# Optimization experiments

Hardware: AMD Instinct MI355X
Metric: run time of the kernel (lower is better)

## Reference

```python
import jax, jax.numpy as jnp
import numpy as np


def setup_inputs() -> dict:
    key = jax.random.key(0)
    ks = jax.random.split(key, 10)
    T, D, E, K, H = 16384, 1024, 8, 2, 4096
    scale = 0.02
    return {
        "x_flat": jax.random.normal(ks[0], (T, D), jnp.float32),
        "noise": jax.random.normal(ks[1], (T, E), jnp.float32),
        "gate_w": jax.random.normal(ks[2], (E, D), jnp.float32) * scale,
        "noise_weight": jnp.zeros((E,), jnp.float32),
        "w1": jax.random.normal(ks[3], (E, H, D), jnp.float32) * scale,
        "b1": jnp.zeros((E, H), jnp.float32),
        "w2": jax.random.normal(ks[4], (E, H, D), jnp.float32) * scale,
        "b2": jnp.zeros((E, H), jnp.float32),
        "wp": jax.random.normal(ks[5], (E, D, H), jnp.float32) * scale,
        "bp": jnp.zeros((E, D), jnp.float32),
    }


K_TOP = 2
LOAD_BALANCE_SCALE = 0.01


def reference(x_flat, noise, gate_w, noise_weight, w1, b1, w2, b2, wp, bp):
    T, D = x_flat.shape
    E = gate_w.shape[0]
    # ---- gate ----
    logits = x_flat @ gate_w.T                        # [T, E]
    gate_weights = jax.nn.softmax(logits, axis=-1)    # [T, E]
    gw_mean = gate_weights.mean(axis=0)               # [E]
    uniform = jnp.ones_like(gw_mean) / E
    load_balance_loss = jnp.mean((gw_mean - uniform) ** 2) * LOAD_BALANCE_SCALE
    # noisy top-k (noise_weight initialized to zeros => noise is a no-op, kept for faithfulness)
    logits_noisy = logits + noise * noise_weight
    top_v, top_i = jax.lax.top_k(logits_noisy, K_TOP)  # [T, K]
    neg_inf = jnp.full_like(logits_noisy, -jnp.inf)
    sparse = neg_inf.at[jnp.arange(T)[:, None], top_i].set(top_v)
    top_k_gated_weights = jax.nn.softmax(sparse, axis=-1)  # [T, E], zero off top-k
    # ---- experts (SwiGLU), weighted combine ----
    # Non-top-k weights are exactly 0, so a dense masked sum over experts equals
    # the original gather/grouped-GEMM/scatter dispatch on a single device.
    y = jnp.zeros_like(x_flat)
    for e in range(E):
        h = x_flat @ w1[e].T + b1[e]                  # [T, H]
        g = jax.nn.silu(x_flat @ w2[e].T + b2[e])     # [T, H]
        out_e = (h * g) @ wp[e].T + bp[e]             # [T, D]
        y = y + top_k_gated_weights[:, e:e + 1] * out_e
    return y, load_balance_loss
```

## Files before the change

kernel.cpp:

```cpp
#include <hip/hip_runtime.h>
#include <hip/hip_bf16.h>

#define T_TOK 16384
#define DDIM  1024
#define NEXP  8
#define HDIM  4096
#define HQ    1024
#define NQ    4
#define TOTR  (2 * T_TOK)

#define BM 128
#define BK 64

typedef __attribute__((ext_vector_type(8))) short bf16x8;
typedef __attribute__((ext_vector_type(4))) float f32x4;

__device__ __forceinline__ unsigned short f2bf(float f) {
  unsigned int x = __builtin_bit_cast(unsigned int, f);
  x += 0x7fffu + ((x >> 16) & 1u);
  return (unsigned short)(x >> 16);
}
__device__ __forceinline__ void gload16(void* lds, const void* g) {
  __builtin_amdgcn_global_load_lds(
      (const __attribute__((address_space(1))) unsigned int*)g,
      (__attribute__((address_space(3))) unsigned int*)lds, 16, 0, 0);
}
__device__ __forceinline__ f32x4 mfma16(bf16x8 a, bf16x8 b, f32x4 c) {
  return __builtin_amdgcn_mfma_f32_16x16x32_bf16(a, b, c, 0, 0, 0);
}

#define OFF_GWSUM  ((size_t)0)
#define OFF_OFF16  ((size_t)64)
#define OFF_NP     ((size_t)128)
#define OFF_BLK    ((size_t)1024)
#define OFF_GBASE  ((size_t)8192)
#define OFF_PEXPP  ((size_t)16384)
#define OFF_PM0P   ((size_t)18432)
#define OFF_PENDP  ((size_t)20480)
#define OFF_PEXPS  ((size_t)22528)
#define OFF_PM0S   ((size_t)24576)
#define OFF_PENDS  ((size_t)26624)
#define OFF_TOPE   ((size_t)32768)
#define OFF_TOPW   (OFF_TOPE   + (size_t)T_TOK*2*4)
#define OFF_LRANK  (OFF_TOPW   + (size_t)T_TOK*2*4)
#define OFF_ROWTOK (OFF_LRANK  + (size_t)T_TOK*4)
#define OFF_ROWG   (OFF_ROWTOK + (size_t)T_TOK*2*4)
#define OFF_XG     ((size_t)1 << 20)
#define OFF_ACTQ   (OFF_XG   + (size_t)TOTR*DDIM*2)
#define OFF_W1Q    (OFF_ACTQ + (size_t)TOTR*HQ*2)
#define OFF_W2Q    (OFF_W1Q  + (size_t)NEXP*HQ*DDIM*2)
#define OFF_WPQ    (OFF_W2Q  + (size_t)NEXP*HQ*DDIM*2)
#define WS_NEEDED  (OFF_WPQ  + (size_t)NEXP*DDIM*HQ*2 + ((size_t)1<<20))

__global__ __launch_bounds__(256) void k_gate(
    const float* __restrict__ x, const float* __restrict__ noise,
    const float* __restrict__ gate_w, const float* __restrict__ nw,
    float* __restrict__ gwsum, int* __restrict__ tope, float* __restrict__ topw)
{
  __shared__ float gw_s[NEXP * DDIM];
  __shared__ float blk_gw[NEXP];
  const int tid = threadIdx.x;
  if (tid < NEXP) blk_gw[tid] = 0.f;
  {
    float4* dst = (float4*)gw_s;
    const float4* src = (const float4*)gate_w;
    for (int i = tid; i < NEXP * DDIM / 4; i += 256) dst[i] = src[i];
  }
  __syncthreads();

  const int wv = tid >> 6, lane = tid & 63;
  const int t = blockIdx.x * 4 + wv;

  const float4* xr = (const float4*)(x + (size_t)t * DDIM);
  float4 xv[4];
  #pragma unroll
  for (int c = 0; c < 4; ++c) xv[c] = xr[lane + 64 * c];

  float logit[NEXP];
  #pragma unroll
  for (int e = 0; e < NEXP; ++e) {
    float p = 0.f;
    const float4* g4 = (const float4*)(gw_s + e * DDIM);
    #pragma unroll
    for (int c = 0; c < 4; ++c) {
      float4 g = g4[lane + 64 * c];
      p += xv[c].x * g.x + xv[c].y * g.y + xv[c].z * g.z + xv[c].w * g.w;
    }
    #pragma unroll
    for (int off = 32; off >= 1; off >>= 1) p += __shfl_xor(p, off, 64);
    logit[e] = p;
  }

  if (lane == 0) {
    float m = logit[0];
    #pragma unroll
    for (int e = 1; e < NEXP; ++e) m = fmaxf(m, logit[e]);
    float sm[NEXP]; float s = 0.f;
    #pragma unroll
    for (int e = 0; e < NEXP; ++e) { sm[e] = expf(logit[e] - m); s += sm[e]; }
    float inv = 1.f / s;
    #pragma unroll
    for (int e = 0; e < NEXP; ++e) atomicAdd(&blk_gw[e], sm[e] * inv);

    float ln[NEXP];
    #pragma unroll
    for (int e = 0; e < NEXP; ++e) ln[e] = logit[e] + noise[(size_t)t * NEXP + e] * nw[e];
    int i1 = 0; float v1 = ln[0];
    #pragma unroll
    for (int e = 1; e < NEXP; ++e) if (ln[e] > v1) { v1 = ln[e]; i1 = e; }
    int i2 = -1; float v2 = -3.4e38f;
    #pragma unroll
    for (int e = 0; e < NEXP; ++e) if (e != i1 && ln[e] > v2) { v2 = ln[e]; i2 = e; }
    float b = expf(v2 - v1);
    float wsum = 1.f + b;
    tope[2 * t] = i1; tope[2 * t + 1] = i2;
    topw[2 * t] = 1.f / wsum; topw[2 * t + 1] = b / wsum;
  }
  __syncthreads();
  if (tid < NEXP) atomicAdd(&gwsum[tid], blk_gw[tid]);
}

__global__ __launch_bounds__(256) void k_hist(
    const int* __restrict__ tope, unsigned int* __restrict__ lrank,
    int* __restrict__ blkcnt)
{
  __shared__ int cnt16[16];
  const int tid = threadIdx.x;
  const int t = blockIdx.x * 256 + tid;
  if (tid < 16) cnt16[tid] = 0;
  __syncthreads();
  const int e0 = tope[2 * t], e1 = tope[2 * t + 1];
  const int b0 = 2 * e0 + (e0 < e1 ? 0 : 1);
  const int b1 = 2 * e1 + (e1 < e0 ? 0 : 1);
  const int lr0 = atomicAdd(&cnt16[b0], 1);
  const int lr1 = atomicAdd(&cnt16[b1], 1);
  lrank[t] = (unsigned int)lr0 | ((unsigned int)lr1 << 16);
  __syncthreads();
  if (tid < 16) blkcnt[blockIdx.x * 16 + tid] = cnt16[tid];
}

__global__ __launch_bounds__(512) void k_scan(
    const int* __restrict__ blkcnt, int* __restrict__ gbase,
    int* __restrict__ off16, int* __restrict__ np,
    int* __restrict__ pexpP, int* __restrict__ pm0P, int* __restrict__ pendP,
    int* __restrict__ pexpS, int* __restrict__ pm0S, int* __restrict__ pendS,
    const float* __restrict__ gwsum, float* __restrict__ out_loss)
{
  __shared__ int ld[64][16];
  __shared__ int sc[64][16];
  __shared__ int tot[16];
  __shared__ int o16[16];
  const int tid = threadIdx.x;
  for (int i = tid; i < 1024; i += 512) ld[i >> 4][i & 15] = blkcnt[i];
  __syncthreads();
  if (tid < 16) {
    int run = 0;
    for (int i = 0; i < 64; ++i) { sc[i][tid] = run; run += ld[i][tid]; }
    tot[tid] = run;
  }
  __syncthreads();
  if (tid == 0) {
    int o = 0;
    for (int b = 0; b < 16; ++b) { o16[b] = o; off16[b] = o; o += tot[b]; }
    int nP = 0, nS = 0;
    for (int b = 0; b < 16; ++b) {
      const int e = b >> 1, s = b & 1;
      const int beg = o16[b], end = beg + tot[b];
      for (int m = beg; m < end; m += BM) {
        const int me = (m + BM < end) ? (m + BM) : end;
        if (!s) { pexpP[nP] = e; pm0P[nP] = m; pendP[nP] = me; ++nP; }
        else    { pexpS[nS] = e; pm0S[nS] = m; pendS[nS] = me; ++nS; }
      }
    }
    np[0] = nP; np[1] = nS;
    float s = 0.f;
    for (int i = 0; i < NEXP; ++i) {
      float d = gwsum[i] / (float)T_TOK - 1.f / (float)NEXP;
      s += d * d;
    }
    out_loss[0] = (s / (float)NEXP) * 0.01f;
  }
  __syncthreads();
  for (int i = tid; i < 1024; i += 512)
    gbase[i] = o16[i & 15] + sc[i >> 4][i & 15];
}

__global__ __launch_bounds__(256) void k_copy(
    const float* __restrict__ x, const int* __restrict__ tope,
    const float* __restrict__ topw, const unsigned int* __restrict__ lrank,
    const int* __restrict__ gbase,
    int* __restrict__ rowtok, float* __restrict__ rowgate,
    unsigned short* __restrict__ Xg)
{
  const int tid = threadIdx.x;
  const int wv = tid >> 6, lane = tid & 63;
  const int t = blockIdx.x * 4 + wv;
  const int e0 = tope[2 * t], e1 = tope[2 * t + 1];
  const int b0 = 2 * e0 + (e0 < e1 ? 0 : 1);
  const int b1 = 2 * e1 + (e1 < e0 ? 0 : 1);
  const unsigned int lr = lrank[t];
  const int hb = t >> 8;
  const int r0 = gbase[hb * 16 + b0] + (int)(lr & 0xffffu);
  const int r1 = gbase[hb * 16 + b1] + (int)(lr >> 16);
  if (lane == 0) {
    rowtok[r0] = t; rowtok[r1] = t;
    rowgate[r0] = topw[2 * t]; rowgate[r1] = topw[2 * t + 1];
  }
  const float4* xr = (const float4*)(x + (size_t)t * DDIM);
  ushort4 o[4];
  #pragma unroll
  for (int c = 0; c < 4; ++c) {
    float4 v = xr[lane + 64 * c];
    o[c].x = f2bf(v.x); o[c].y = f2bf(v.y); o[c].z = f2bf(v.z); o[c].w = f2bf(v.w);
  }
  ushort4* d0 = (ushort4*)(Xg + (size_t)r0 * DDIM);
  ushort4* d1 = (ushort4*)(Xg + (size_t)r1 * DDIM);
  #pragma unroll
  for (int c = 0; c < 4; ++c) d0[lane + 64 * c] = o[c];
  #pragma unroll
  for (int c = 0; c < 4; ++c) d1[lane + 64 * c] = o[c];
}

__global__ __launch_bounds__(256) void k_castall(
    const float* __restrict__ w1, const float* __restrict__ w2,
    const float* __restrict__ wp,
    unsigned short* __restrict__ w1q, unsigned short* __restrict__ w2q,
    unsigned short* __restrict__ wpq, int q)
{
  const int N4 = NEXP * HQ * DDIM / 4;
  for (int i = blockIdx.x * 256 + threadIdx.x; i < 3 * N4; i += gridDim.x * 256) {
    int j = i;
    float4 v; size_t dstIdx; unsigned short* d;
    if (j < N4) {
      const int c4 = j & 255, rr = j >> 8, e = rr >> 10, r = rr & 1023;
      v = ((const float4*)w1)[((size_t)e * HDIM + q * HQ + r) * 256 + c4];
      d = w1q; dstIdx = (size_t)rr * 256 + c4;
    } else if (j < 2 * N4) {
      j -= N4;
      const int c4 = j & 255, rr = j >> 8, e = rr >> 10, r = rr & 1023;
      v = ((const float4*)w2)[((size_t)e * HDIM + q * HQ + r) * 256 + c4];
      d = w2q; dstIdx = (size_t)rr * 256 + c4;
    } else {
      j -= 2 * N4;
      const int c4 = j & 255, rr = j >> 8;
      v = ((const float4*)wp)[(size_t)rr * 1024 + q * 256 + c4];
      d = wpq; dstIdx = (size_t)rr * 256 + c4;
    }
    ushort4 o;
    o.x = f2bf(v.x); o.y = f2bf(v.y); o.z = f2bf(v.z); o.w = f2bf(v.w);
    ((ushort4*)d)[dstIdx] = o;
  }
}

#define FBN 64
#define FGX 280
#define FGY 16
__global__ __launch_bounds__(256, 2) void k_fused(
    const unsigned short* __restrict__ Xg,
    const unsigned short* __restrict__ w1q, const unsigned short* __restrict__ w2q,
    const float* __restrict__ b1, const float* __restrict__ b2,
    unsigned short* __restrict__ actq, const int* __restrict__ np,
    const int* __restrict__ pexpP, const int* __restrict__ pm0P, const int* __restrict__ pendP,
    const int* __restrict__ pexpS, const int* __restrict__ pm0S, const int* __restrict__ pendS,
    int q)
{
  const int flat = blockIdx.y * FGX + blockIdx.x;
  const int CPX = (FGX * FGY) / 8;
  const int L = (flat & 7) * CPX + (flat >> 3);
  const int pidx = L >> 4;
  const int yc = L & 15;
  const int nP = np[0], nS = np[1];
  int e, m0, mend;
  if (pidx < nP)            { e = pexpP[pidx]; m0 = pm0P[pidx]; mend = pendP[pidx]; }
  else if (pidx < nP + nS)  { int s = pidx - nP; e = pexpS[s]; m0 = pm0S[s]; mend = pendS[s]; }
  else return;

  __shared__ unsigned short As[2][BM * BK];
  __shared__ unsigned short B1s[2][FBN * BK];
  __shared__ unsigned short B2s[2][FBN * BK];

  const int tid = threadIdx.x;
  const int wid = tid >> 6, lane = tid & 63;
  const int wr = wid >> 1, wc = wid & 1;
  const int fr = lane & 15;
  const int fq = lane >> 4;

  const unsigned short* Bbase1 = w1q + ((size_t)e * HQ + yc * FBN) * DDIM;
  const unsigned short* Bbase2 = w2q + ((size_t)e * HQ + yc * FBN) * DDIM;

  f32x4 acc1[4][2] = {};
  f32x4 acc2[4][2] = {};

  auto stage = [&](int kt, int cur) {
    const int k0 = kt * BK;
    #pragma unroll
    for (int it = 0; it < 4; ++it) {
      const int idx = it * 256 + tid;
      const int row = idx >> 3, seg = idx & 7;
      const int koff = ((seg ^ (row & 7)) << 3);
      int arow = m0 + row; if (arow >= TOTR) arow = TOTR - 1;
      gload16(&As[cur][idx * 8], Xg + (size_t)arow * DDIM + k0 + koff);
    }
    #pragma unroll
    for (int it = 0; it < 2; ++it) {
      const int idx = it * 256 + tid;
      const int row = idx >> 3, seg = idx & 7;
      const int koff = ((seg ^ (row & 7)) << 3);
      gload16(&B1s[cur][idx * 8], Bbase1 + (size_t)row * DDIM + k0 + koff);
    }
    #pragma unroll
    for (int it = 0; it < 2; ++it) {
      const int idx = it * 256 + tid;
      const int row = idx >> 3, seg = idx & 7;
      const int koff = ((seg ^ (row & 7)) << 3);
      gload16(&B2s[cur][idx * 8], Bbase2 + (size_t)row * DDIM + k0 + koff);
    }
  };

  const int NSTEP = DDIM / BK;
  stage(0, 0);

  for (int kt = 0; kt < NSTEP; ++kt) {
    const int cur = kt & 1;
    const bool has_next = (kt + 1 < NSTEP);
    if (has_next) stage(kt + 1, cur ^ 1);
    if (has_next) asm volatile("s_waitcnt vmcnt(8)" ::: "memory");
    else          asm volatile("s_waitcnt vmcnt(0)" ::: "memory");
    __builtin_amdgcn_sched_barrier(0);
    __builtin_amdgcn_s_barrier();
    __builtin_amdgcn_s_setprio(1);

    #pragma unroll
    for (int kk = 0; kk < 2; ++kk) {
      bf16x8 b1v[2], b2v[2];
      #pragma unroll
      for (int nf = 0; nf < 2; ++nf) {
        const int row = wc * 32 + nf * 16 + fr;
        const int seg = (kk * 4 + fq) ^ (row & 7);
        b1v[nf] = *(const bf16x8*)&B1s[cur][row * BK + seg * 8];
        b2v[nf] = *(const bf16x8*)&B2s[cur][row * BK + seg * 8];
      }
      #pragma unroll
      for (int mf = 0; mf < 4; ++mf) {
        const int row = wr * 64 + mf * 16 + fr;
        const int seg = (kk * 4 + fq) ^ (row & 7);
        bf16x8 av = *(const bf16x8*)&As[cur][row * BK + seg * 8];
        #pragma unroll
        for (int nf = 0; nf < 2; ++nf) {
          acc1[mf][nf] = mfma16(av, b1v[nf], acc1[mf][nf]);
          acc2[mf][nf] = mfma16(av, b2v[nf], acc2[mf][nf]);
        }
      }
    }

    __builtin_amdgcn_s_setprio(0);
    __builtin_amdgcn_s_barrier();
    __builtin_amdgcn_sched_barrier(0);
  }

  const int mcnt = mend - m0;
  #pragma unroll
  for (int mf = 0; mf < 4; ++mf) {
    const int rb = wr * 64 + mf * 16 + (fq << 2);
    #pragma unroll
    for (int nf = 0; nf < 2; ++nf) {
      const int cq = yc * FBN + wc * 32 + nf * 16 + fr;
      const float bb1 = b1[(size_t)e * HDIM + q * HQ + cq];
      const float bb2 = b2[(size_t)e * HDIM + q * HQ + cq];
      #pragma unroll
      for (int j = 0; j < 4; ++j) {
        const int lr = rb + j;
        if (lr < mcnt) {
          float h = acc1[mf][nf][j] + bb1;
          float g = acc2[mf][nf][j] + bb2;
          float s = g / (1.f + expf(-g));
          actq[(size_t)(m0 + lr) * HQ + cq] = f2bf(h * s);
        }
      }
    }
  }
}

#define DBN 64
#define DGX 144
#define DGY 16
template<bool STORE>
__global__ __launch_bounds__(256, 2) void k_down(
    const unsigned short* __restrict__ actq, const unsigned short* __restrict__ wpq,
    const float* __restrict__ bp,
    const int* __restrict__ np, int npIdx,
    const int* __restrict__ pexp, const int* __restrict__ pm0, const int* __restrict__ pend,
    const int* __restrict__ rowtok, const float* __restrict__ rowgate,
    float* __restrict__ Y)
{
  const int flat = blockIdx.y * DGX + blockIdx.x;
  const int CPX = (DGX * DGY) / 8;
  const int L = (flat & 7) * CPX + (flat >> 3);
  const int pidx = L >> 4;
  const int yc = L & 15;
  if (pidx >= np[npIdx]) return;
  const int e = pexp[pidx], m0 = pm0[pidx], mend = pend[pidx];

  __shared__ unsigned short As[2][BM * BK];
  __shared__ unsigned short Bs[2][DBN * BK];

  const int tid = threadIdx.x;
  const int wid = tid >> 6, lane = tid & 63;
  const int wr = wid >> 1, wc = wid & 1;
  const int fr = lane & 15;
  const int fq = lane >> 4;

  const unsigned short* Bbase = wpq + ((size_t)e * DDIM + yc * DBN) * HQ;

  f32x4 acc[4][2] = {};

  auto stage = [&](int kt, int cur) {
    const int k0 = kt * BK;
    #pragma unroll
    for (int it = 0; it < 4; ++it) {
      const int idx = it * 256 + tid;
      const int row = idx >> 3, seg = idx & 7;
      const int koff = ((seg ^ (row & 7)) << 3);
      int arow = m0 + row; if (arow >= TOTR) arow = TOTR - 1;
      gload16(&As[cur][idx * 8], actq + (size_t)arow * HQ + k0 + koff);
    }
    #pragma unroll
    for (int it = 0; it < 2; ++it) {
      const int idx = it * 256 + tid;
      const int row = idx >> 3, seg = idx & 7;
      const int koff = ((seg ^ (row & 7)) << 3);
      gload16(&Bs[cur][idx * 8], Bbase + (size_t)row * HQ + k0 + koff);
    }
  };

  const int NSTEP = HQ / BK;
  stage(0, 0);

  for (int kt = 0; kt < NSTEP; ++kt) {
    const int cur = kt & 1;
    const bool has_next = (kt + 1 < NSTEP);
    if (has_next) stage(kt + 1, cur ^ 1);
    if (has_next) asm volatile("s_waitcnt vmcnt(6)" ::: "memory");
    else          asm volatile("s_waitcnt vmcnt(0)" ::: "memory");
    __builtin_amdgcn_sched_barrier(0);
    __builtin_amdgcn_s_barrier();
    __builtin_amdgcn_s_setprio(1);

    #pragma unroll
    for (int kk = 0; kk < 2; ++kk) {
      bf16x8 bv[2];
      #pragma unroll
      for (int nf = 0; nf < 2; ++nf) {
        const int row = wc * 32 + nf * 16 + fr;
        const int seg = (kk * 4 + fq) ^ (row & 7);
        bv[nf] = *(const bf16x8*)&Bs[cur][row * BK + seg * 8];
      }
      #pragma unroll
      for (int mf = 0; mf < 4; ++mf) {
        const int row = wr * 64 + mf * 16 + fr;
        const int seg = (kk * 4 + fq) ^ (row & 7);
        bf16x8 av = *(const bf16x8*)&As[cur][row * BK + seg * 8];
        #pragma unroll
        for (int nf = 0; nf < 2; ++nf)
          acc[mf][nf] = mfma16(av, bv[nf], acc[mf][nf]);
      }
    }

    __builtin_amdgcn_s_setprio(0);
    __builtin_amdgcn_s_barrier();
    __builtin_amdgcn_sched_barrier(0);
  }

  const int mcnt = mend - m0;
  #pragma unroll
  for (int mf = 0; mf < 4; ++mf) {
    const int rb = wr * 64 + mf * 16 + (fq << 2);
    #pragma unroll
    for (int nf = 0; nf < 2; ++nf) {
      const int dg = yc * DBN + wc * 32 + nf * 16 + fr;
      const float bb = bp[(size_t)e * DDIM + dg];
      #pragma unroll
      for (int j = 0; j < 4; ++j) {
        const int lr = rb + j;
        if (lr < mcnt) {
          const int r = m0 + lr;
          const float o = rowgate[r] * (acc[mf][nf][j] + bb);
          float* yp = &Y[(size_t)rowtok[r] * DDIM + dg];
          if (STORE) *yp = o; else *yp += o;
        }
      }
    }
  }
}

extern "C" void kernel_launch(void* const* d_in, const int* in_sizes, int n_in,
                              void* d_out, int out_size, void* d_ws, size_t ws_size,
                              hipStream_t stream) {
  const float* x      = (const float*)d_in[0];
  const float* noise  = (const float*)d_in[1];
  const float* gate_w = (const float*)d_in[2];
  const float* nw     = (const float*)d_in[3];
  const float* w1     = (const float*)d_in[4];
  const float* b1     = (const float*)d_in[5];
  const float* w2     = (const float*)d_in[6];
  const float* b2     = (const float*)d_in[7];
  const float* wp     = (const float*)d_in[8];
  const float* bp     = (const float*)d_in[9];
  float* y = (float*)d_out;

  if (ws_size < WS_NEEDED) return;

  char* ws = (char*)d_ws;
  float* gwsum   = (float*)(ws + OFF_GWSUM);
  int*   off16   = (int*)(ws + OFF_OFF16);
  int*   np      = (int*)(ws + OFF_NP);
  int*   blkcnt  = (int*)(ws + OFF_BLK);
  int*   gbase   = (int*)(ws + OFF_GBASE);
  int*   pexpP   = (int*)(ws + OFF_PEXPP);
  int*   pm0P    = (int*)(ws + OFF_PM0P);
  int*   pendP   = (int*)(ws + OFF_PENDP);
  int*   pexpS   = (int*)(ws + OFF_PEXPS);
  int*   pm0S    = (int*)(ws + OFF_PM0S);
  int*   pendS   = (int*)(ws + OFF_PENDS);
  int*   tope    = (int*)(ws + OFF_TOPE);
  float* topw    = (float*)(ws + OFF_TOPW);
  unsigned int* lrank = (unsigned int*)(ws + OFF_LRANK);
  int*   rowtok  = (int*)(ws + OFF_ROWTOK);
  float* rowgate = (float*)(ws + OFF_ROWG);
  unsigned short* Xg   = (unsigned short*)(ws + OFF_XG);
  unsigned short* actq = (unsigned short*)(ws + OFF_ACTQ);
  unsigned short* w1q  = (unsigned short*)(ws + OFF_W1Q);
  unsigned short* w2q  = (unsigned short*)(ws + OFF_W2Q);
  unsigned short* wpq  = (unsigned short*)(ws + OFF_WPQ);

  hipMemsetAsync(d_ws, 0, 64, stream);

  k_gate<<<T_TOK / 4, 256, 0, stream>>>(x, noise, gate_w, nw, gwsum, tope, topw);
  k_hist<<<T_TOK / 256, 256, 0, stream>>>(tope, lrank, blkcnt);
  k_scan<<<1, 512, 0, stream>>>(blkcnt, gbase, off16, np,
                                pexpP, pm0P, pendP, pexpS, pm0S, pendS,
                                gwsum, y + (size_t)T_TOK * DDIM);
  k_copy<<<T_TOK / 4, 256, 0, stream>>>(x, tope, topw, lrank, gbase,
                                        rowtok, rowgate, Xg);

  for (int q = 0; q < NQ; ++q) {
    k_castall<<<3072, 256, 0, stream>>>(w1, w2, wp, w1q, w2q, wpq, q);
    k_fused<<<dim3(FGX, FGY), 256, 0, stream>>>(
        Xg, w1q, w2q, b1, b2, actq, np,
        pexpP, pm0P, pendP, pexpS, pm0S, pendS, q);
    if (q == 0)
      k_down<true><<<dim3(DGX, DGY), 256, 0, stream>>>(
          actq, wpq, bp, np, 0, pexpP, pm0P, pendP, rowtok, rowgate, y);
    else
      k_down<false><<<dim3(DGX, DGY), 256, 0, stream>>>(
          actq, wpq, bp, np, 0, pexpP, pm0P, pendP, rowtok, rowgate, y);
    k_down<false><<<dim3(DGX, DGY), 256, 0, stream>>>(
        actq, wpq, bp, np, 1, pexpS, pm0S, pendS, rowtok, rowgate, y);
  }
}
```

Measured before the change: 2.063 ms.

## Drop double-buffering in FFN kernels and widen down-proj tile to 128 columns

Both the fused up/gate kernel and the down-projection kernel go from double-buffered async LDS staging with manual waitcnt and priority hints to single-buffered tiles with __syncthreads around each load. The down kernel now has each block compute two 64-column output halves (128 columns), halving the grid's y dimension so each activation tile loaded into LDS feeds twice as much MFMA work. The trade is that global loads no longer overlap compute and a block needs more accumulator registers, which may cost occupancy, in exchange for less LDS use and fewer activation reloads.

```diff
diff --git a/kernel.cpp b/kernel.cpp
--- a/kernel.cpp
+++ b/kernel.cpp
@@ -275,9 +275,9 @@
   else if (pidx < nP + nS)  { int s = pidx - nP; e = pexpS[s]; m0 = pm0S[s]; mend = pendS[s]; }
   else return;
 
-  __shared__ unsigned short As[2][BM * BK];
-  __shared__ unsigned short B1s[2][FBN * BK];
-  __shared__ unsigned short B2s[2][FBN * BK];
+  __shared__ unsigned short As[BM * BK];
+  __shared__ unsigned short B1s[FBN * BK];
+  __shared__ unsigned short B2s[FBN * BK];
 
   const int tid = threadIdx.x;
   const int wid = tid >> 6, lane = tid & 63;
@@ -291,7 +291,8 @@
   f32x4 acc1[4][2] = {};
   f32x4 acc2[4][2] = {};
 
-  auto stage = [&](int kt, int cur) {
+  for (int kt = 0; kt < DDIM / BK; ++kt) {
+    if (kt > 0) __syncthreads();
     const int k0 = kt * BK;
     #pragma unroll
     for (int it = 0; it < 4; ++it) {
@@ -299,36 +300,23 @@
       const int row = idx >> 3, seg = idx & 7;
       const int koff = ((seg ^ (row & 7)) << 3);
       int arow = m0 + row; if (arow >= TOTR) arow = TOTR - 1;
-      gload16(&As[cur][idx * 8], Xg + (size_t)arow * DDIM + k0 + koff);
+      gload16(&As[idx * 8], Xg + (size_t)arow * DDIM + k0 + koff);
     }
     #pragma unroll
     for (int it = 0; it < 2; ++it) {
       const int idx = it * 256 + tid;
       const int row = idx >> 3, seg = idx & 7;
       const int koff = ((seg ^ (row & 7)) << 3);
-      gload16(&B1s[cur][idx * 8], Bbase1 + (size_t)row * DDIM + k0 + koff);
+      gload16(&B1s[idx * 8], Bbase1 + (size_t)row * DDIM + k0 + koff);
     }
     #pragma unroll
     for (int it = 0; it < 2; ++it) {
       const int idx = it * 256 + tid;
       const int row = idx >> 3, seg = idx & 7;
       const int koff = ((seg ^ (row & 7)) << 3);
-      gload16(&B2s[cur][idx * 8], Bbase2 + (size_t)row * DDIM + k0 + koff);
-    }
-  };
-
-  const int NSTEP = DDIM / BK;
-  stage(0, 0);
-
-  for (int kt = 0; kt < NSTEP; ++kt) {
-    const int cur = kt & 1;
-    const bool has_next = (kt + 1 < NSTEP);
-    if (has_next) stage(kt + 1, cur ^ 1);
-    if (has_next) asm volatile("s_waitcnt vmcnt(8)" ::: "memory");
-    else          asm volatile("s_waitcnt vmcnt(0)" ::: "memory");
-    __builtin_amdgcn_sched_barrier(0);
-    __builtin_amdgcn_s_barrier();
-    __builtin_amdgcn_s_setprio(1);
+      gload16(&B2s[idx * 8], Bbase2 + (size_t)row * DDIM + k0 + koff);
+    }
+    __syncthreads();
 
     #pragma unroll
     for (int kk = 0; kk < 2; ++kk) {
@@ -337,14 +325,14 @@
       for (int nf = 0; nf < 2; ++nf) {
         const int row = wc * 32 + nf * 16 + fr;
         const int seg = (kk * 4 + fq) ^ (row & 7);
-        b1v[nf] = *(const bf16x8*)&B1s[cur][row * BK + seg * 8];
-        b2v[nf] = *(const bf16x8*)&B2s[cur][row * BK + seg * 8];
+        b1v[nf] = *(const bf16x8*)&B1s[row * BK + seg * 8];
+        b2v[nf] = *(const bf16x8*)&B2s[row * BK + seg * 8];
       }
       #pragma unroll
       for (int mf = 0; mf < 4; ++mf) {
         const int row = wr * 64 + mf * 16 + fr;
         const int seg = (kk * 4 + fq) ^ (row & 7);
-        bf16x8 av = *(const bf16x8*)&As[cur][row * BK + seg * 8];
+        bf16x8 av = *(const bf16x8*)&As[row * BK + seg * 8];
         #pragma unroll
         for (int nf = 0; nf < 2; ++nf) {
           acc1[mf][nf] = mfma16(av, b1v[nf], acc1[mf][nf]);
@@ -352,10 +340,6 @@
         }
       }
     }
-
-    __builtin_amdgcn_s_setprio(0);
-    __builtin_amdgcn_s_barrier();
-    __builtin_amdgcn_sched_barrier(0);
   }
 
   const int mcnt = mend - m0;
@@ -383,7 +367,7 @@
 
 #define DBN 64
 #define DGX 144
-#define DGY 16
+#define DGY 8
 template<bool STORE>
 __global__ __launch_bounds__(256, 2) void k_down(
     const unsigned short* __restrict__ actq, const unsigned short* __restrict__ wpq,
@@ -396,13 +380,14 @@
   const int flat = blockIdx.y * DGX + blockIdx.x;
   const int CPX = (DGX * DGY) / 8;
   const int L = (flat & 7) * CPX + (flat >> 3);
-  const int pidx = L >> 4;
-  const int yc = L & 15;
+  const int pidx = L >> 3;
+  const int yc = L & 7;
   if (pidx >= np[npIdx]) return;
   const int e = pexp[pidx], m0 = pm0[pidx], mend = pend[pidx];
 
-  __shared__ unsigned short As[2][BM * BK];
-  __shared__ unsigned short Bs[2][DBN * BK];
+  __shared__ unsigned short As[BM * BK];
+  __shared__ unsigned short Bs1[DBN * BK];
+  __shared__ unsigned short Bs2[DBN * BK];
 
   const int tid = threadIdx.x;
   const int wid = tid >> 6, lane = tid & 63;
@@ -410,11 +395,14 @@
   const int fr = lane & 15;
   const int fq = lane >> 4;
 
-  const unsigned short* Bbase = wpq + ((size_t)e * DDIM + yc * DBN) * HQ;
-
-  f32x4 acc[4][2] = {};
-
-  auto stage = [&](int kt, int cur) {
+  const unsigned short* Bbase1 = wpq + ((size_t)e * DDIM + yc * 128) * HQ;
+  const unsigned short* Bbase2 = Bbase1 + (size_t)64 * HQ;
+
+  f32x4 acc1[4][2] = {};
+  f32x4 acc2[4][2] = {};
+
+  for (int kt = 0; kt < HQ / BK; ++kt) {
+    if (kt > 0) __syncthreads();
     const int k0 = kt * BK;
     #pragma unroll
     for (int it = 0; it < 4; ++it) {
@@ -422,53 +410,46 @@
       const int row = idx >> 3, seg = idx & 7;
       const int koff = ((seg ^ (row & 7)) << 3);
       int arow = m0 + row; if (arow >= TOTR) arow = TOTR - 1;
-      gload16(&As[cur][idx * 8], actq + (size_t)arow * HQ + k0 + koff);
+      gload16(&As[idx * 8], actq + (size_t)arow * HQ + k0 + koff);
     }
     #pragma unroll
     for (int it = 0; it < 2; ++it) {
       const int idx = it * 256 + tid;
       const int row = idx >> 3, seg = idx & 7;
       const int koff = ((seg ^ (row & 7)) << 3);
-      gload16(&Bs[cur][idx * 8], Bbase + (size_t)row * HQ + k0 + koff);
-    }
-  };
-
-  const int NSTEP = HQ / BK;
-  stage(0, 0);
-
-  for (int kt = 0; kt < NSTEP; ++kt) {
-    const int cur = kt & 1;
-    const bool has_next = (kt + 1 < NSTEP);
-    if (has_next) stage(kt + 1, cur ^ 1);
-    if (has_next) asm volatile("s_waitcnt vmcnt(6)" ::: "memory");
-    else          asm volatile("s_waitcnt vmcnt(0)" ::: "memory");
-    __builtin_amdgcn_sched_barrier(0);
-    __builtin_amdgcn_s_barrier();
-    __builtin_amdgcn_s_setprio(1);
+      gload16(&Bs1[idx * 8], Bbase1 + (size_t)row * HQ + k0 + koff);
+    }
+    #pragma unroll
+    for (int it = 0; it < 2; ++it) {
+      const int idx = it * 256 + tid;
+      const int row = idx >> 3, seg = idx & 7;
+      const int koff = ((seg ^ (row & 7)) << 3);
+      gload16(&Bs2[idx * 8], Bbase2 + (size_t)row * HQ + k0 + koff);
+    }
+    __syncthreads();
 
     #pragma unroll
     for (int kk = 0; kk < 2; ++kk) {
-      bf16x8 bv[2];
+      bf16x8 b1v[2], b2v[2];
       #pragma unroll
       for (int nf = 0; nf < 2; ++nf) {
         const int row = wc * 32 + nf * 16 + fr;
         const int seg = (kk * 4 + fq) ^ (row & 7);
-        bv[nf] = *(const bf16x8*)&Bs[cur][row * BK + seg * 8];
+        b1v[nf] = *(const bf16x8*)&Bs1[row * BK + seg * 8];
+        b2v[nf] = *(const bf16x8*)&Bs2[row * BK + seg * 8];
       }
       #pragma unroll
       for (int mf = 0; mf < 4; ++mf) {
         const int row = wr * 64 + mf * 16 + fr;
         const int seg = (kk * 4 + fq) ^ (row & 7);
-        bf16x8 av = *(const bf16x8*)&As[cur][row * BK + seg * 8];
+        bf16x8 av = *(const bf16x8*)&As[row * BK + seg * 8];
         #pragma unroll
-        for (int nf = 0; nf < 2; ++nf)
-          acc[mf][nf] = mfma16(av, bv[nf], acc[mf][nf]);
-      }
-    }
-
-    __builtin_amdgcn_s_setprio(0);
-    __builtin_amdgcn_s_barrier();
-    __builtin_amdgcn_sched_barrier(0);
+        for (int nf = 0; nf < 2; ++nf) {
+          acc1[mf][nf] = mfma16(av, b1v[nf], acc1[mf][nf]);
+          acc2[mf][nf] = mfma16(av, b2v[nf], acc2[mf][nf]);
+        }
+      }
+    }
   }
 
   const int mcnt = mend - m0;
@@ -477,16 +458,21 @@
     const int rb = wr * 64 + mf * 16 + (fq << 2);
     #pragma unroll
     for (int nf = 0; nf < 2; ++nf) {
-      const int dg = yc * DBN + wc * 32 + nf * 16 + fr;
-      const float bb = bp[(size_t)e * DDIM + dg];
+      const int dg1 = yc * 128 + wc * 32 + nf * 16 + fr;
+      const int dg2 = dg1 + 64;
+      const float bb1 = bp[(size_t)e * DDIM + dg1];
+      const float bb2 = bp[(size_t)e * DDIM + dg2];
       #pragma unroll
       for (int j = 0; j < 4; ++j) {
         const int lr = rb + j;
         if (lr < mcnt) {
           const int r = m0 + lr;
-          const float o = rowgate[r] * (acc[mf][nf][j] + bb);
-          float* yp = &Y[(size_t)rowtok[r] * DDIM + dg];
-          if (STORE) *yp = o; else *yp += o;
+          const float gt = rowgate[r];
+          float* yrow = &Y[(size_t)rowtok[r] * DDIM];
+          const float o1 = gt * (acc1[mf][nf][j] + bb1);
+          const float o2 = gt * (acc2[mf][nf][j] + bb2);
+          if (STORE) { yrow[dg1] = o1; yrow[dg2] = o2; }
+          else       { yrow[dg1] += o1; yrow[dg2] += o2; }
         }
       }
     }
```

Result: faster. 1.663 ms, median of 2 (-19.4%).
